# Optimization experiments

Measured on AMD Instinct MI355X. Metric: run time of the kernel, lower is better.

The kernel has to match this reference:

```python
import jax, jax.numpy as jnp
import numpy as np

NEG = -1e30

def setup_inputs() -> dict:
    key = jax.random.key(0)
    k = jax.random.split(key, 6)
    B, Lc, Lq, D = 16, 2048, 256, 256
    c = jax.random.normal(k[0], (B, Lc, D), dtype=jnp.float32)
    q = jax.random.normal(k[1], (B, Lq, D), dtype=jnp.float32)
    c_mask = jnp.ones((B, Lc), dtype=jnp.float32)
    q_mask = jnp.ones((B, Lq), dtype=jnp.float32)
    # xavier-uniform-ish scale for the similarity weights
    lim = float(np.sqrt(6.0 / (D + 1)))
    cq_weight = jax.random.uniform(k[2], (1, 1, D), jnp.float32, -lim, lim)
    c_weight = jax.random.uniform(k[3], (1, D), jnp.float32, -lim, lim)
    q_weight = jax.random.uniform(k[4], (1, D), jnp.float32, -lim, lim)
    bias = jnp.zeros((1,), dtype=jnp.float32)
    return {"c": c, "q": q, "c_mask": c_mask, "q_mask": q_mask,
            "cq_weight": cq_weight, "c_weight": c_weight,
            "q_weight": q_weight, "bias": bias}

def _masked_softmax(logits, mask):
    # mask: 1=keep, 0=pad; broadcast over logits' leading dims
    x = logits * mask + (1.0 - mask) * NEG
    return jax.nn.softmax(x, axis=-1)

def reference(c, q, c_mask, q_mask, cq_weight, c_weight, q_weight, bias):
    # trilinear similarity S[b,i,j] = w_c.c_i + w_q.q_j + (c_i*w_cq).q_j + b
    s0 = jnp.einsum('bid,od->bio', c, c_weight)              # [B,Lc,1]
    s1 = jnp.einsum('bjd,od->boj', q, q_weight)              # [B,1,Lq]
    s2 = jnp.einsum('bid,bjd->bij', c * cq_weight, q)        # [B,Lc,Lq]
    S = s0 + s1 + s2 + bias                                  # [B,Lc,Lq]
    S1 = _masked_softmax(S, q_mask[:, None, :])              # softmax over q
    C2Q = jnp.einsum('bij,bjd->bid', S1, q)                  # [B,Lc,D]
    S2t = _masked_softmax(jnp.swapaxes(S, 1, 2), c_mask[:, None, :])  # [B,Lq,Lc]
    S2 = jnp.einsum('bij,bjk->bik', S1, S2t)                 # [B,Lc,Lc]
    Q2C = jnp.einsum('bik,bkd->bid', S2, c)                  # [B,Lc,D]
    return jnp.concatenate((c, C2Q, c * C2Q, c * Q2C), axis=-1)
```

## Files before the change

### kernel.cpp

```cpp
#include <hip/hip_runtime.h>
#include <hip/hip_bf16.h>

#define NB 16
#define LC 2048
#define LQ 256
#define DD 256
#define NEGINF -1e30f

typedef __attribute__((ext_vector_type(8))) short bf16x8;
typedef __attribute__((ext_vector_type(4))) float f32x4;

#define MFMA16(a, b, c) __builtin_amdgcn_mfma_f32_16x16x32_bf16((a), (b), (c), 0, 0, 0)

typedef const unsigned int __attribute__((address_space(1))) glb_u32;
typedef unsigned int __attribute__((address_space(3))) lds_u32;

__device__ __forceinline__ void gload_lds16(const void* g, void* l) {
    __builtin_amdgcn_global_load_lds((glb_u32*)g, (lds_u32*)l, 16, 0, 0);
}

__device__ __forceinline__ short f2b(float x) {
    unsigned u = __float_as_uint(x);
    unsigned r = (u + 0x7fffu + ((u >> 16) & 1u)) >> 16;
    return (short)r;
}
__device__ __forceinline__ float b2f(short s) {
    return __uint_as_float(((unsigned)(unsigned short)s) << 16);
}

#define NCB (NB * LC / 8)
__global__ __launch_bounds__(256) void prep(
        const float* __restrict__ c, const float* __restrict__ q,
        const float* __restrict__ c_w, const float* __restrict__ cqw,
        const float* __restrict__ q_w, const float* __restrict__ bias,
        short* __restrict__ c16, float* __restrict__ s0c,
        short* __restrict__ qw16, short* __restrict__ qT16,
        float* __restrict__ s1q, float* __restrict__ out) {
    __shared__ float T[64][65];
    int t = threadIdx.x;
    if (blockIdx.x < NCB) {
        int row = blockIdx.x * 8 + (t >> 5);
        int k = t & 31;
        const float* src = c + (size_t)row * DD + k * 8;
        float4 v0 = *(const float4*)(src);
        float4 v1 = *(const float4*)(src + 4);
        float4 w0 = *(const float4*)(c_w + k * 8);
        float4 w1 = *(const float4*)(c_w + k * 8 + 4);
        float s = v0.x * w0.x + v0.y * w0.y + v0.z * w0.z + v0.w * w0.w
                + v1.x * w1.x + v1.y * w1.y + v1.z * w1.z + v1.w * w1.w;
        #pragma unroll
        for (int o = 16; o > 0; o >>= 1) s += __shfl_xor(s, o, 64);
        if (k == 0) s0c[row] = s;
        size_t ob = (size_t)row * (size_t)(4 * DD) + k * 8;
        *(float4*)(out + ob)     = v0;
        *(float4*)(out + ob + 4) = v1;
        ushort4 o0, o1;
        o0.x = (unsigned short)f2b(v0.x); o0.y = (unsigned short)f2b(v0.y);
        o0.z = (unsigned short)f2b(v0.z); o0.w = (unsigned short)f2b(v0.w);
        o1.x = (unsigned short)f2b(v1.x); o1.y = (unsigned short)f2b(v1.y);
        o1.z = (unsigned short)f2b(v1.z); o1.w = (unsigned short)f2b(v1.w);
        ushort4* dst = (ushort4*)(c16 + (size_t)row * DD + k * 8);
        dst[0] = o0;
        dst[1] = o1;
    } else {
        int idx = blockIdx.x - NCB;
        int b = idx >> 2, j0 = (idx & 3) * 64;
        int dd = t & 63, rg = t >> 6;
        float acc[16];
        #pragma unroll
        for (int i = 0; i < 16; ++i) acc[i] = 0.f;
        for (int dc = 0; dc < 4; ++dc) {
            float wv = cqw[dc * 64 + dd];
            float qwv = q_w[dc * 64 + dd];
            #pragma unroll
            for (int rr = 0; rr < 16; ++rr) {
                int r = rg + 4 * rr;
                float v = q[((size_t)b * LQ + j0 + r) * DD + dc * 64 + dd];
                qw16[((size_t)b * LQ + j0 + r) * DD + dc * 64 + dd] = f2b(v * wv);
                acc[rr] += v * qwv;
                T[dd][r] = v;
            }
            __syncthreads();
            int jj = t & 63;
            for (int dw = t >> 6; dw < 64; dw += 4)
                qT16[((size_t)b * DD + dc * 64 + dw) * LQ + j0 + jj] = f2b(T[dw][jj]);
            __syncthreads();
        }
        float bv = bias[0];
        #pragma unroll
        for (int rr = 0; rr < 16; ++rr) {
            float s = acc[rr];
            #pragma unroll
            for (int o = 32; o > 0; o >>= 1) s += __shfl_xor(s, o, 64);
            if (dd == 0) s1q[b * LQ + j0 + rg + 4 * rr] = s + bv;
        }
    }
}

__global__ __launch_bounds__(512) void k1_S(
        const short* __restrict__ c16, const short* __restrict__ qw16,
        const float* __restrict__ cmask, const float* __restrict__ qmask,
        const float* __restrict__ s0c, const float* __restrict__ s1q,
        short* __restrict__ P1b, float* __restrict__ wgtg,
        float* __restrict__ pm, float* __restrict__ ps) {
    __shared__ short As[128 * 64];
    __shared__ short Bs[256 * 64];
    __shared__ float rmLds[128 * 4];
    __shared__ float rsLds[128 * 4];
    __shared__ float rowCLds[128];
    int b  = blockIdx.y;
    int i0 = blockIdx.x * 128;
    int t = threadIdx.x;
    int l = t & 63, w = t >> 6;
    int wr = w >> 2, wc = w & 3;

    f32x4 acc[4][4];
    #pragma unroll
    for (int m = 0; m < 4; ++m)
        #pragma unroll
        for (int n = 0; n < 4; ++n) acc[m][n] = (f32x4){0.f, 0.f, 0.f, 0.f};

    const short* Ag = c16  + ((size_t)b * LC + i0) * DD;
    const short* Bg = qw16 + ((size_t)b * LQ) * DD;
    int lrow = l >> 3;
    int lcolsw = ((l & 7) ^ lrow) * 8;

    for (int kt = 0; kt < DD; kt += 64) {
        __syncthreads();
        #pragma unroll
        for (int r = 0; r < 2; ++r) {
            int chunk = r * 8 + w;
            int row = chunk * 8 + lrow;
            gload_lds16(Ag + (size_t)row * DD + kt + lcolsw, As + chunk * 512);
        }
        #pragma unroll
        for (int r = 0; r < 4; ++r) {
            int chunk = r * 8 + w;
            int row = chunk * 8 + lrow;
            gload_lds16(Bg + (size_t)row * DD + kt + lcolsw, Bs + chunk * 512);
        }
        __syncthreads();
        #pragma unroll
        for (int kf = 0; kf < 2; ++kf) {
            bf16x8 a[4], bb[4];
            #pragma unroll
            for (int m = 0; m < 4; ++m) {
                int row = wr * 64 + m * 16 + (l & 15);
                int byte = row * 128 + kf * 64 + (l >> 4) * 16;
                a[m] = *(const bf16x8*)((const char*)As + (byte ^ ((row & 7) << 4)));
            }
            #pragma unroll
            for (int n = 0; n < 4; ++n) {
                int row = wc * 64 + n * 16 + (l & 15);
                int byte = row * 128 + kf * 64 + (l >> 4) * 16;
                bb[n] = *(const bf16x8*)((const char*)Bs + (byte ^ ((row & 7) << 4)));
            }
            #pragma unroll
            for (int m = 0; m < 4; ++m)
                #pragma unroll
                for (int n = 0; n < 4; ++n)
                    acc[m][n] = MFMA16(a[m], bb[n], acc[m][n]);
        }
    }

    float s1v[4], qmv[4], negq[4];
    #pragma unroll
    for (int n = 0; n < 4; ++n) {
        int j = wc * 64 + n * 16 + (l & 15);
        s1v[n] = s1q[b * LQ + j];
        qmv[n] = qmask[b * LQ + j];
        negq[n] = (1.f - qmv[n]) * NEGINF;
    }
    float s0r[4][4], cmr[4][4];
    #pragma unroll
    for (int m = 0; m < 4; ++m)
        #pragma unroll
        for (int reg = 0; reg < 4; ++reg) {
            int il = wr * 64 + m * 16 + (l >> 4) * 4 + reg;
            s0r[m][reg] = s0c[b * LC + i0 + il];
            cmr[m][reg] = cmask[b * LC + i0 + il];
        }
    #pragma unroll
    for (int m = 0; m < 4; ++m)
        #pragma unroll
        for (int n = 0; n < 4; ++n)
            #pragma unroll
            for (int reg = 0; reg < 4; ++reg)
                acc[m][n][reg] = acc[m][n][reg] + s0r[m][reg] + s1v[n];

    #pragma unroll
    for (int n = 0; n < 4; ++n) {
        float x2v[16];
        float mx = NEGINF;
        #pragma unroll
        for (int m = 0; m < 4; ++m)
            #pragma unroll
            for (int reg = 0; reg < 4; ++reg) {
                float cm = cmr[m][reg];
                float x2 = acc[m][n][reg] * cm + (1.f - cm) * NEGINF;
                x2v[m * 4 + reg] = x2;
                mx = fmaxf(mx, x2);
            }
        float ss = 0.f;
        #pragma unroll
        for (int e = 0; e < 16; ++e) ss += __expf(x2v[e] - mx);
        #pragma unroll
        for (int off = 16; off <= 32; off <<= 1) {
            float om = __shfl_xor(mx, off, 64);
            float os = __shfl_xor(ss, off, 64);
            float nm = fmaxf(mx, om);
            ss = ss * __expf(mx - nm) + os * __expf(om - nm);
            mx = nm;
        }
        if (l < 16) {
            size_t idx = ((size_t)b * 32 + blockIdx.x * 2 + wr) * LQ + wc * 64 + n * 16 + l;
            pm[idx] = mx;
            ps[idx] = ss;
        }
    }

    #pragma unroll
    for (int m = 0; m < 4; ++m)
        #pragma unroll
        for (int reg = 0; reg < 4; ++reg) {
            float mx = NEGINF;
            #pragma unroll
            for (int n = 0; n < 4; ++n)
                mx = fmaxf(mx, fmaf(acc[m][n][reg], qmv[n], negq[n]));
            #pragma unroll
            for (int o = 1; o <= 8; o <<= 1) mx = fmaxf(mx, __shfl_xor(mx, o, 64));
            float ss = 0.f;
            #pragma unroll
            for (int n = 0; n < 4; ++n)
                ss += __expf(fmaf(acc[m][n][reg], qmv[n], negq[n]) - mx);
            #pragma unroll
            for (int o = 1; o <= 8; o <<= 1) ss += __shfl_xor(ss, o, 64);
            if ((l & 15) == 0) {
                int row = wr * 64 + m * 16 + (l >> 4) * 4 + reg;
                rmLds[row * 4 + wc] = mx;
                rsLds[row * 4 + wc] = ss;
            }
        }
    __syncthreads();
    if (t < 128) {
        float m0 = rmLds[t * 4 + 0], m1 = rmLds[t * 4 + 1];
        float m2 = rmLds[t * 4 + 2], m3 = rmLds[t * 4 + 3];
        float mm = fmaxf(fmaxf(m0, m1), fmaxf(m2, m3));
        float ss = rsLds[t * 4 + 0] * __expf(m0 - mm)
                 + rsLds[t * 4 + 1] * __expf(m1 - mm)
                 + rsLds[t * 4 + 2] * __expf(m2 - mm)
                 + rsLds[t * 4 + 3] * __expf(m3 - mm);
        float rc = mm + logf(ss);
        rowCLds[t] = rc;
        wgtg[(size_t)b * LC + i0 + t] = cmask[b * LC + i0 + t] * __expf(rc);
    }
    __syncthreads();

    float rCv[4][4];
    #pragma unroll
    for (int m = 0; m < 4; ++m)
        #pragma unroll
        for (int reg = 0; reg < 4; ++reg)
            rCv[m][reg] = rowCLds[wr * 64 + m * 16 + (l >> 4) * 4 + reg];
    #pragma unroll
    for (int m = 0; m < 4; ++m)
        #pragma unroll
        for (int n = 0; n < 4; ++n)
            #pragma unroll
            for (int reg = 0; reg < 4; ++reg) {
                float p = __expf(fmaf(acc[m][n][reg], qmv[n], negq[n]) - rCv[m][reg]);
                int il = wr * 64 + m * 16 + (l >> 4) * 4 + reg;
                int j = wc * 64 + n * 16 + (l & 15);
                P1b[((size_t)b * LC + i0 + il) * LQ + j] = f2b(p);
            }
}

#define K3S 72
__global__ __launch_bounds__(256) void k3_A2C(
        const short* __restrict__ c16, const short* __restrict__ P1b,
        const float* __restrict__ wgtg,
        float* __restrict__ p3) {
    __shared__ short As[128 * K3S];
    __shared__ short Bs[128 * K3S];
    int b  = blockIdx.z;
    int ks = blockIdx.y;
    int d0 = (blockIdx.x >> 1) * 128;
    int j0 = (blockIdx.x & 1) * 128;
    int t = threadIdx.x, l = t & 63, w = t >> 6;
    int wr = w >> 1, wc = w & 1;

    f32x4 acc[4][4];
    #pragma unroll
    for (int m = 0; m < 4; ++m)
        #pragma unroll
        for (int n = 0; n < 4; ++n) acc[m][n] = (f32x4){0.f, 0.f, 0.f, 0.f};

    int ii4 = (t >> 4) * 4;
    int c8  = (t & 15) * 8;
    int ip  = ii4 ^ (((c8 >> 3) & 7) << 3);

    for (int k0 = ks * 512; k0 < ks * 512 + 512; k0 += 64) {
        __syncthreads();
        bf16x8 av[4], pv[4];
        float wv[4];
        #pragma unroll
        for (int r = 0; r < 4; ++r) {
            size_t gi = (size_t)b * LC + k0 + ii4 + r;
            av[r] = *(const bf16x8*)(c16 + gi * DD + d0 + c8);
            pv[r] = *(const bf16x8*)(P1b + gi * LQ + j0 + c8);
            wv[r] = wgtg[gi];
        }
        #pragma unroll
        for (int g = 0; g < 8; ++g) {
            short4 a4, b4;
            a4.x = av[0][g]; a4.y = av[1][g]; a4.z = av[2][g]; a4.w = av[3][g];
            b4.x = f2b(b2f(pv[0][g]) * wv[0]);
            b4.y = f2b(b2f(pv[1][g]) * wv[1]);
            b4.z = f2b(b2f(pv[2][g]) * wv[2]);
            b4.w = f2b(b2f(pv[3][g]) * wv[3]);
            *(short4*)(&As[(c8 + g) * K3S + ip]) = a4;
            *(short4*)(&Bs[(c8 + g) * K3S + ip]) = b4;
        }
        __syncthreads();
        #pragma unroll
        for (int kf = 0; kf < 2; ++kf) {
            bf16x8 a[4], bb[4];
            int colL = kf * 32 + (l >> 4) * 8;
            #pragma unroll
            for (int m = 0; m < 4; ++m) {
                int row = wr * 64 + m * 16 + (l & 15);
                int colP = colL ^ (((row >> 3) & 7) << 3);
                a[m] = *(const bf16x8*)((const char*)As +
                        row * (K3S * 2) + colP * 2);
            }
            #pragma unroll
            for (int n = 0; n < 4; ++n) {
                int row = wc * 64 + n * 16 + (l & 15);
                int colP = colL ^ (((row >> 3) & 7) << 3);
                bb[n] = *(const bf16x8*)((const char*)Bs +
                        row * (K3S * 2) + colP * 2);
            }
            #pragma unroll
            for (int m = 0; m < 4; ++m)
                #pragma unroll
                for (int n = 0; n < 4; ++n)
                    acc[m][n] = MFMA16(a[m], bb[n], acc[m][n]);
        }
    }
    float* P = p3 + (((size_t)b * 4 + ks) * 4 + blockIdx.x) * 16384;
    #pragma unroll
    for (int m = 0; m < 4; ++m)
        #pragma unroll
        for (int n = 0; n < 4; ++n)
            #pragma unroll
            for (int reg = 0; reg < 4; ++reg) {
                int ld = wr * 64 + m * 16 + (l >> 4) * 4 + reg;
                int lj = wc * 64 + n * 16 + (l & 15);
                P[ld * 128 + lj] = acc[m][n][reg];
            }
}

__global__ __launch_bounds__(256) void k3r_reduce(
        const float* __restrict__ p3,
        const float* __restrict__ pm, const float* __restrict__ ps,
        short* __restrict__ A2CT) {
    __shared__ float colCs[256];
    int b = blockIdx.y;
    int t = threadIdx.x;
    {
        float m = NEGINF, s = 0.f;
        for (int ch = 0; ch < 32; ++ch) {
            float pmv = pm[((size_t)b * 32 + ch) * LQ + t];
            float psv = ps[((size_t)b * 32 + ch) * LQ + t];
            float mn = fmaxf(m, pmv);
            s = s * __expf(m - mn) + psv * __expf(pmv - mn);
            m = mn;
        }
        colCs[t] = m + logf(s);
    }
    __syncthreads();
    int linear = blockIdx.x * 256 + t;
    int d = linear >> 6;
    int j4 = (linear & 63) * 4;
    int tile = (d >> 7) * 2 + (j4 >> 7);
    int ld = d & 127, lj = j4 & 127;
    const float* base = p3 + (((size_t)b * 4) * 4 + tile) * 16384 + ld * 128 + lj;
    float4 s = {0.f, 0.f, 0.f, 0.f};
    #pragma unroll
    for (int ks = 0; ks < 4; ++ks) {
        float4 v = *(const float4*)(base + (size_t)ks * 4 * 16384);
        s.x += v.x; s.y += v.y; s.z += v.z; s.w += v.w;
    }
    s.x *= __expf(-colCs[j4 + 0]);
    s.y *= __expf(-colCs[j4 + 1]);
    s.z *= __expf(-colCs[j4 + 2]);
    s.w *= __expf(-colCs[j4 + 3]);
    short4 o;
    o.x = f2b(s.x); o.y = f2b(s.y); o.z = f2b(s.z); o.w = f2b(s.w);
    *(short4*)(A2CT + ((size_t)b * DD + d) * LQ + j4) = o;
}

__global__ __launch_bounds__(256) void k4_out(
        const short* __restrict__ P1b, const short* __restrict__ qT16,
        const short* __restrict__ A2CT, const short* __restrict__ c16,
        float* __restrict__ out) {
    __shared__ float Lo1[16][260];
    __shared__ float Lo2[16][260];
    int b = blockIdx.y, i0 = blockIdx.x * 64;
    int t = threadIdx.x, l = t & 63, w = t >> 6;
    int d0w = w * 64;

    f32x4 acc1[4][4], acc2[4][4];
    #pragma unroll
    for (int m = 0; m < 4; ++m)
        #pragma unroll
        for (int n = 0; n < 4; ++n) {
            acc1[m][n] = (f32x4){0.f, 0.f, 0.f, 0.f};
            acc2[m][n] = (f32x4){0.f, 0.f, 0.f, 0.f};
        }
    const short* Sr  = P1b  + ((size_t)b * LC + i0) * LQ;
    const short* qTb = qT16 + (size_t)b * DD * LQ;
    const short* aTb = A2CT + (size_t)b * DD * LQ;

    #pragma unroll 2
    for (int kf = 0; kf < 8; ++kf) {
        int j8 = kf * 32 + (l >> 4) * 8;
        bf16x8 a[4];
        #pragma unroll
        for (int m = 0; m < 4; ++m)
            a[m] = *(const bf16x8*)(Sr + (size_t)(m * 16 + (l & 15)) * LQ + j8);
        #pragma unroll
        for (int n = 0; n < 4; ++n) {
            int d = d0w + n * 16 + (l & 15);
            size_t off = (size_t)d * LQ + j8;
            bf16x8 bq = *(const bf16x8*)(qTb + off);
            bf16x8 ba = *(const bf16x8*)(aTb + off);
            #pragma unroll
            for (int m = 0; m < 4; ++m) {
                acc1[m][n] = MFMA16(a[m], bq, acc1[m][n]);
                acc2[m][n] = MFMA16(a[m], ba, acc2[m][n]);
            }
        }
    }

    const short* cb16 = c16 + (size_t)b * LC * DD;
    #pragma unroll
    for (int m = 0; m < 4; ++m) {
        __syncthreads();
        #pragma unroll
        for (int n = 0; n < 4; ++n) {
            int col = d0w + n * 16 + (l & 15);
            #pragma unroll
            for (int reg = 0; reg < 4; ++reg) {
                int row = (l >> 4) * 4 + reg;
                Lo1[row][col] = acc1[m][n][reg];
                Lo2[row][col] = acc2[m][n][reg];
            }
        }
        __syncthreads();
        #pragma unroll
        for (int rr = 0; rr < 4; ++rr) {
            int row = w * 4 + rr;
            int i = i0 + m * 16 + row;
            float4 f1 = *(const float4*)&Lo1[row][l * 4];
            float4 f2 = *(const float4*)&Lo2[row][l * 4];
            short4 cu = *(const short4*)(cb16 + (size_t)i * DD + l * 4);
            float c0 = b2f(cu.x), c1 = b2f(cu.y), c2 = b2f(cu.z), c3 = b2f(cu.w);
            size_t ob = ((size_t)b * LC + i) * (size_t)(4 * DD);
            float4 p1 = {c0 * f1.x, c1 * f1.y, c2 * f1.z, c3 * f1.w};
            float4 p2 = {c0 * f2.x, c1 * f2.y, c2 * f2.z, c3 * f2.w};
            *(float4*)(out + ob + 256 + l * 4) = f1;
            *(float4*)(out + ob + 512 + l * 4) = p1;
            *(float4*)(out + ob + 768 + l * 4) = p2;
        }
    }
}

extern "C" void kernel_launch(void* const* d_in, const int* in_sizes, int n_in,
                              void* d_out, int out_size, void* d_ws, size_t ws_size,
                              hipStream_t stream) {
    const float* c     = (const float*)d_in[0];
    const float* q     = (const float*)d_in[1];
    const float* cmask = (const float*)d_in[2];
    const float* qmask = (const float*)d_in[3];
    const float* cqw   = (const float*)d_in[4];
    const float* c_w   = (const float*)d_in[5];
    const float* q_w   = (const float*)d_in[6];
    const float* bias  = (const float*)d_in[7];
    float* out = (float*)d_out;

    char* w = (char*)d_ws;
    short* P1b   = (short*)(w);
    short* c16   = (short*)(w + 16777216);
    short* qw16  = (short*)(w + 33554432);
    short* qT16  = (short*)(w + 35651584);
    short* A2CT  = (short*)(w + 37748736);
    float* s0c   = (float*)(w + 39845888);
    float* s1q   = (float*)(w + 39976960);
    float* pm    = (float*)(w + 39993344);
    float* ps    = (float*)(w + 40517632);
    float* wgtg  = (float*)(w + 41041920);
    float* p3    = (float*)(w + 41172992);

    prep<<<dim3(NCB + NB * LQ / 64), dim3(256), 0, stream>>>(
        c, q, c_w, cqw, q_w, bias, c16, s0c, qw16, qT16, s1q, out);
    k1_S<<<dim3(LC / 128, NB), dim3(512), 0, stream>>>(
        c16, qw16, cmask, qmask, s0c, s1q, P1b, wgtg, pm, ps);
    k3_A2C<<<dim3(4, 4, NB), dim3(256), 0, stream>>>(
        c16, P1b, wgtg, p3);
    k3r_reduce<<<dim3(64, NB), dim3(256), 0, stream>>>(p3, pm, ps, A2CT);
    k4_out<<<dim3(LC / 64, NB), dim3(256), 0, stream>>>(
        P1b, qT16, A2CT, c16, out);
}
```

Baseline: 117.9 us.

## Fuse c conversion, s0 dot product and output copy into the S kernel

The c-side preprocessing (bf16 conversion, the c_w dot product and copying c into the first output slice) moves out of the prep kernel and into k1_S. k1_S now reads fp32 c directly, converts it into LDS, writes c16 and out, and reduces s0 locally through LDS. The prep kernel shrinks to the q-side work only. This removes one full read of c and the s0c round trip through global memory. In exchange the A-tile loads in k1_S become synchronous register loads rather than direct global-to-LDS loads, and k1_S does more per-block global writes.

```diff
diff --git a/kernel.cpp b/kernel.cpp
--- a/kernel.cpp
+++ b/kernel.cpp
@@ -28,86 +28,59 @@
     return __uint_as_float(((unsigned)(unsigned short)s) << 16);
 }
 
-#define NCB (NB * LC / 8)
-__global__ __launch_bounds__(256) void prep(
-        const float* __restrict__ c, const float* __restrict__ q,
-        const float* __restrict__ c_w, const float* __restrict__ cqw,
+__global__ __launch_bounds__(256) void prep_q(
+        const float* __restrict__ q, const float* __restrict__ cqw,
         const float* __restrict__ q_w, const float* __restrict__ bias,
-        short* __restrict__ c16, float* __restrict__ s0c,
         short* __restrict__ qw16, short* __restrict__ qT16,
-        float* __restrict__ s1q, float* __restrict__ out) {
+        float* __restrict__ s1q) {
     __shared__ float T[64][65];
-    int t = threadIdx.x;
-    if (blockIdx.x < NCB) {
-        int row = blockIdx.x * 8 + (t >> 5);
-        int k = t & 31;
-        const float* src = c + (size_t)row * DD + k * 8;
-        float4 v0 = *(const float4*)(src);
-        float4 v1 = *(const float4*)(src + 4);
-        float4 w0 = *(const float4*)(c_w + k * 8);
-        float4 w1 = *(const float4*)(c_w + k * 8 + 4);
-        float s = v0.x * w0.x + v0.y * w0.y + v0.z * w0.z + v0.w * w0.w
-                + v1.x * w1.x + v1.y * w1.y + v1.z * w1.z + v1.w * w1.w;
-        #pragma unroll
-        for (int o = 16; o > 0; o >>= 1) s += __shfl_xor(s, o, 64);
-        if (k == 0) s0c[row] = s;
-        size_t ob = (size_t)row * (size_t)(4 * DD) + k * 8;
-        *(float4*)(out + ob)     = v0;
-        *(float4*)(out + ob + 4) = v1;
-        ushort4 o0, o1;
-        o0.x = (unsigned short)f2b(v0.x); o0.y = (unsigned short)f2b(v0.y);
-        o0.z = (unsigned short)f2b(v0.z); o0.w = (unsigned short)f2b(v0.w);
-        o1.x = (unsigned short)f2b(v1.x); o1.y = (unsigned short)f2b(v1.y);
-        o1.z = (unsigned short)f2b(v1.z); o1.w = (unsigned short)f2b(v1.w);
-        ushort4* dst = (ushort4*)(c16 + (size_t)row * DD + k * 8);
-        dst[0] = o0;
-        dst[1] = o1;
-    } else {
-        int idx = blockIdx.x - NCB;
-        int b = idx >> 2, j0 = (idx & 3) * 64;
-        int dd = t & 63, rg = t >> 6;
-        float acc[16];
-        #pragma unroll
-        for (int i = 0; i < 16; ++i) acc[i] = 0.f;
-        for (int dc = 0; dc < 4; ++dc) {
-            float wv = cqw[dc * 64 + dd];
-            float qwv = q_w[dc * 64 + dd];
-            #pragma unroll
-            for (int rr = 0; rr < 16; ++rr) {
-                int r = rg + 4 * rr;
-                float v = q[((size_t)b * LQ + j0 + r) * DD + dc * 64 + dd];
-                qw16[((size_t)b * LQ + j0 + r) * DD + dc * 64 + dd] = f2b(v * wv);
-                acc[rr] += v * qwv;
-                T[dd][r] = v;
-            }
-            __syncthreads();
-            int jj = t & 63;
-            for (int dw = t >> 6; dw < 64; dw += 4)
-                qT16[((size_t)b * DD + dc * 64 + dw) * LQ + j0 + jj] = f2b(T[dw][jj]);
-            __syncthreads();
-        }
-        float bv = bias[0];
+    int b = blockIdx.y, j0 = blockIdx.x * 64, t = threadIdx.x;
+    int dd = t & 63, rg = t >> 6;
+    float acc[16];
+    #pragma unroll
+    for (int i = 0; i < 16; ++i) acc[i] = 0.f;
+    for (int dc = 0; dc < 4; ++dc) {
+        float wv = cqw[dc * 64 + dd];
+        float qwv = q_w[dc * 64 + dd];
         #pragma unroll
         for (int rr = 0; rr < 16; ++rr) {
-            float s = acc[rr];
-            #pragma unroll
-            for (int o = 32; o > 0; o >>= 1) s += __shfl_xor(s, o, 64);
-            if (dd == 0) s1q[b * LQ + j0 + rg + 4 * rr] = s + bv;
-        }
+            int r = rg + 4 * rr;
+            float v = q[((size_t)b * LQ + j0 + r) * DD + dc * 64 + dd];
+            qw16[((size_t)b * LQ + j0 + r) * DD + dc * 64 + dd] = f2b(v * wv);
+            acc[rr] += v * qwv;
+            T[dd][r] = v;
+        }
+        __syncthreads();
+        int jj = t & 63;
+        for (int dw = t >> 6; dw < 64; dw += 4)
+            qT16[((size_t)b * DD + dc * 64 + dw) * LQ + j0 + jj] = f2b(T[dw][jj]);
+        __syncthreads();
+    }
+    float bv = bias[0];
+    #pragma unroll
+    for (int rr = 0; rr < 16; ++rr) {
+        float s = acc[rr];
+        #pragma unroll
+        for (int o = 32; o > 0; o >>= 1) s += __shfl_xor(s, o, 64);
+        if (dd == 0) s1q[b * LQ + j0 + rg + 4 * rr] = s + bv;
     }
 }
 
 __global__ __launch_bounds__(512) void k1_S(
-        const short* __restrict__ c16, const short* __restrict__ qw16,
+        const float* __restrict__ c, const short* __restrict__ qw16,
+        const float* __restrict__ c_w,
         const float* __restrict__ cmask, const float* __restrict__ qmask,
-        const float* __restrict__ s0c, const float* __restrict__ s1q,
-        short* __restrict__ P1b, float* __restrict__ wgtg,
-        float* __restrict__ pm, float* __restrict__ ps) {
+        const float* __restrict__ s1q,
+        short* __restrict__ c16, short* __restrict__ P1b,
+        float* __restrict__ wgtg,
+        float* __restrict__ pm, float* __restrict__ ps,
+        float* __restrict__ out) {
     __shared__ short As[128 * 64];
     __shared__ short Bs[256 * 64];
     __shared__ float rmLds[128 * 4];
     __shared__ float rsLds[128 * 4];
     __shared__ float rowCLds[128];
+    __shared__ float s0Lds[128];
     int b  = blockIdx.y;
     int i0 = blockIdx.x * 128;
     int t = threadIdx.x;
@@ -120,25 +93,42 @@
         #pragma unroll
         for (int n = 0; n < 4; ++n) acc[m][n] = (f32x4){0.f, 0.f, 0.f, 0.f};
 
-    const short* Ag = c16  + ((size_t)b * LC + i0) * DD;
+    const float* cg = c + ((size_t)b * LC + i0) * DD;
     const short* Bg = qw16 + ((size_t)b * LQ) * DD;
+    short* c16g = c16 + ((size_t)b * LC + i0) * DD;
     int lrow = l >> 3;
     int lcolsw = ((l & 7) ^ lrow) * 8;
+    int csA = (l & 7) ^ lrow;
+    float s0acc[2] = {0.f, 0.f};
 
     for (int kt = 0; kt < DD; kt += 64) {
         __syncthreads();
-        #pragma unroll
-        for (int r = 0; r < 2; ++r) {
-            int chunk = r * 8 + w;
-            int row = chunk * 8 + lrow;
-            gload_lds16(Ag + (size_t)row * DD + kt + lcolsw, As + chunk * 512);
-        }
         #pragma unroll
         for (int r = 0; r < 4; ++r) {
             int chunk = r * 8 + w;
             int row = chunk * 8 + lrow;
             gload_lds16(Bg + (size_t)row * DD + kt + lcolsw, Bs + chunk * 512);
         }
+        #pragma unroll
+        for (int r = 0; r < 2; ++r) {
+            int chunk = r * 8 + w;
+            int row = chunk * 8 + lrow;
+            const float* src = cg + (size_t)row * DD + kt + csA * 8;
+            float4 v0 = *(const float4*)(src);
+            float4 v1 = *(const float4*)(src + 4);
+            float4 w0 = *(const float4*)(c_w + kt + csA * 8);
+            float4 w1 = *(const float4*)(c_w + kt + csA * 8 + 4);
+            s0acc[r] += v0.x * w0.x + v0.y * w0.y + v0.z * w0.z + v0.w * w0.w
+                      + v1.x * w1.x + v1.y * w1.y + v1.z * w1.z + v1.w * w1.w;
+            bf16x8 pk;
+            pk[0] = f2b(v0.x); pk[1] = f2b(v0.y); pk[2] = f2b(v0.z); pk[3] = f2b(v0.w);
+            pk[4] = f2b(v1.x); pk[5] = f2b(v1.y); pk[6] = f2b(v1.z); pk[7] = f2b(v1.w);
+            *(bf16x8*)(As + chunk * 512 + l * 8) = pk;
+            *(bf16x8*)(c16g + (size_t)row * DD + kt + csA * 8) = pk;
+            size_t ob = ((size_t)b * LC + i0 + row) * (size_t)(4 * DD) + kt + csA * 8;
+            *(float4*)(out + ob)     = v0;
+            *(float4*)(out + ob + 4) = v1;
+        }
         __syncthreads();
         #pragma unroll
         for (int kf = 0; kf < 2; ++kf) {
@@ -162,6 +152,16 @@
                     acc[m][n] = MFMA16(a[m], bb[n], acc[m][n]);
         }
     }
+
+    #pragma unroll
+    for (int r = 0; r < 2; ++r) {
+        float s = s0acc[r];
+        s += __shfl_xor(s, 1, 64);
+        s += __shfl_xor(s, 2, 64);
+        s += __shfl_xor(s, 4, 64);
+        if ((l & 7) == 0) s0Lds[(r * 8 + w) * 8 + lrow] = s;
+    }
+    __syncthreads();
 
     float s1v[4], qmv[4], negq[4];
     #pragma unroll
@@ -177,7 +177,7 @@
         #pragma unroll
         for (int reg = 0; reg < 4; ++reg) {
             int il = wr * 64 + m * 16 + (l >> 4) * 4 + reg;
-            s0r[m][reg] = s0c[b * LC + i0 + il];
+            s0r[m][reg] = s0Lds[il];
             cmr[m][reg] = cmask[b * LC + i0 + il];
         }
     #pragma unroll
@@ -330,15 +330,13 @@
             for (int m = 0; m < 4; ++m) {
                 int row = wr * 64 + m * 16 + (l & 15);
                 int colP = colL ^ (((row >> 3) & 7) << 3);
-                a[m] = *(const bf16x8*)((const char*)As +
-                        row * (K3S * 2) + colP * 2);
+                a[m] = *(const bf16x8*)((const char*)As + row * (K3S * 2) + colP * 2);
             }
             #pragma unroll
             for (int n = 0; n < 4; ++n) {
                 int row = wc * 64 + n * 16 + (l & 15);
                 int colP = colL ^ (((row >> 3) & 7) << 3);
-                bb[n] = *(const bf16x8*)((const char*)Bs +
-                        row * (K3S * 2) + colP * 2);
+                bb[n] = *(const bf16x8*)((const char*)Bs + row * (K3S * 2) + colP * 2);
             }
             #pragma unroll
             for (int m = 0; m < 4; ++m)
@@ -495,17 +493,16 @@
     short* qw16  = (short*)(w + 33554432);
     short* qT16  = (short*)(w + 35651584);
     short* A2CT  = (short*)(w + 37748736);
-    float* s0c   = (float*)(w + 39845888);
     float* s1q   = (float*)(w + 39976960);
     float* pm    = (float*)(w + 39993344);
     float* ps    = (float*)(w + 40517632);
     float* wgtg  = (float*)(w + 41041920);
     float* p3    = (float*)(w + 41172992);
 
-    prep<<<dim3(NCB + NB * LQ / 64), dim3(256), 0, stream>>>(
-        c, q, c_w, cqw, q_w, bias, c16, s0c, qw16, qT16, s1q, out);
+    prep_q<<<dim3(LQ / 64, NB), dim3(256), 0, stream>>>(
+        q, cqw, q_w, bias, qw16, qT16, s1q);
     k1_S<<<dim3(LC / 128, NB), dim3(512), 0, stream>>>(
-        c16, qw16, cmask, qmask, s0c, s1q, P1b, wgtg, pm, ps);
+        c, qw16, c_w, cmask, qmask, s1q, c16, P1b, wgtg, pm, ps, out);
     k3_A2C<<<dim3(4, 4, NB), dim3(256), 0, stream>>>(
         c16, P1b, wgtg, p3);
     k3r_reduce<<<dim3(64, NB), dim3(256), 0, stream>>>(p3, pm, ps, A2CT);
```

After: 114.3 us. -3.1%, faster.
